# Performance work log

Hardware: AMD Instinct MI355X
Metric: run time of the kernel (lower is better)

Reference implementation:

```python
import jax, jax.numpy as jnp
import numpy as np

V, D, C, H = 32, 128, 2048, 8
B, M = 8, 2048
HD = D // H


def rms_norm(x, scale):
    # Whole-tensor (per-batch) RMS over dims (1,2), as in the source (quirky but faithful).
    Bx, Mx, Dx = x.shape
    fr = jnp.sqrt(jnp.sum(x * x, axis=(1, 2))) * (Mx * Dx) ** -0.5  # (B,)
    raw = x / fr[:, None, None]
    return scale[:Mx, :][None, :, :] * raw


def rope_tables(Mx):
    i = jnp.arange(D // 2, dtype=jnp.float32)
    # NOTE: faithful to source: exponent uses (i-1), not i.
    base = jnp.power(10000.0, -2.0 * (i - 1.0) / D)  # (D/2,)
    pos = jnp.arange(Mx, dtype=jnp.float32)
    ang = pos[:, None] * base[None, :]  # (M, D/2)
    return jnp.cos(ang), jnp.sin(ang)


def apply_rope(t, cos, sin):
    # Equivalent to bmm with the block-diagonal 2x2 rotation matrices:
    # out[2i]   =  t[2i]*cos + t[2i+1]*sin
    # out[2i+1] = -t[2i]*sin + t[2i+1]*cos
    te, to = t[..., 0::2], t[..., 1::2]
    oe = te * cos + to * sin
    oo = -te * sin + to * cos
    return jnp.stack([oe, oo], axis=-1).reshape(t.shape)


def mha(q, k, v, in_w, in_b, out_w, out_b):
    Bx, Mx, _ = q.shape
    qp = q @ in_w[:D].T + in_b[:D]
    kp = k @ in_w[D:2 * D].T + in_b[D:2 * D]
    vp = v @ in_w[2 * D:].T + in_b[2 * D:]
    qh = qp.reshape(Bx, Mx, H, HD).transpose(0, 2, 1, 3)
    kh = kp.reshape(Bx, Mx, H, HD).transpose(0, 2, 1, 3)
    vh = vp.reshape(Bx, Mx, H, HD).transpose(0, 2, 1, 3)
    scores = jnp.einsum('bhqd,bhkd->bhqk', qh, kh) / jnp.sqrt(jnp.float32(HD))
    causal = jnp.tril(jnp.ones((Mx, Mx), dtype=bool))
    scores = jnp.where(causal[None, None], scores, -jnp.inf)
    probs = jax.nn.softmax(scores, axis=-1)  # dropout=0.1 in train mode; eval here
    o = jnp.einsum('bhqk,bhkd->bhqd', probs, vh)
    o = o.transpose(0, 2, 1, 3).reshape(Bx, Mx, D)
    return o @ out_w.T + out_b


def setup_inputs():
    key = jax.random.key(0)
    ks = jax.random.split(key, 12)
    s = 0.02
    return {
        'idx': jax.random.randint(ks[0], (B, M), 0, V),
        'targets': jax.random.randint(ks[1], (B, M), 0, V),
        'emb': jax.random.normal(ks[2], (V, D), jnp.float32) * s,
        'rms_scale': jnp.ones((C, D), jnp.float32),
        'Wq': jax.random.normal(ks[3], (D, D), jnp.float32) * s,
        'Wk': jax.random.normal(ks[4], (D, D), jnp.float32) * s,
        'Wv': jax.random.normal(ks[5], (D, D), jnp.float32) * s,
        'in_proj_w': jax.random.normal(ks[6], (3 * D, D), jnp.float32) * s,
        'in_proj_b': jnp.zeros((3 * D,), jnp.float32),
        'out_proj_w': jax.random.normal(ks[7], (D, D), jnp.float32) * s,
        'out_proj_b': jnp.zeros((D,), jnp.float32),
        'lin_w': jax.random.normal(ks[8], (D, D), jnp.float32) * s,
        'lin_b': jnp.zeros((D,), jnp.float32),
        'out_w': jax.random.normal(ks[9], (V, D), jnp.float32) * s,
        'out_b': jnp.zeros((V,), jnp.float32),
    }


def reference(idx, targets, emb, rms_scale, Wq, Wk, Wv, in_proj_w, in_proj_b,
              out_proj_w, out_proj_b, lin_w, lin_b, out_w, out_b):
    x = emb[idx]                                  # (B, M, D)
    x = rms_norm(x, rms_scale)
    Q = x @ Wq.T
    K = x @ Wk.T
    Vv = x @ Wv.T
    cos, sin = rope_tables(x.shape[1])
    q_out = apply_rope(Q, cos, sin)
    k_out = apply_rope(K, cos, sin)
    v_out = apply_rope(Vv, cos, sin)              # source rotates V too (faithful)
    x = x + mha(q_out, k_out, v_out, in_proj_w, in_proj_b, out_proj_w, out_proj_b)
    x = rms_norm(x, rms_scale)
    x = x + jax.nn.relu(x @ lin_w.T + lin_b)
    logits = x @ out_w.T + out_b                  # (B, M, V)
    logp = jax.nn.log_softmax(logits, axis=-1)
    nll = -jnp.take_along_axis(logp, targets[..., None], axis=-1)[..., 0]
    loss = jnp.mean(nll)
    return logits, loss
```

## Files before the change

kernel.cpp:

```cpp
#include <hip/hip_runtime.h>
#include <hip/hip_bf16.h>
#include <math.h>

#define Vv   32
#define Dd   128
#define Hh   8
#define Bb   8
#define Mm   2048
#define BM   (Bb*Mm)
#define NEL  (BM*Dd)
#define XNS  140
#define QKS  396

typedef _Float16 half4_t __attribute__((ext_vector_type(4)));
typedef _Float16 half8_t __attribute__((ext_vector_type(8)));
typedef __fp16   fp16x2  __attribute__((ext_vector_type(2)));
typedef float    float4_t __attribute__((ext_vector_type(4)));
#define MFMA16 __builtin_amdgcn_mfma_f32_16x16x16f16

#if __has_builtin(__builtin_amdgcn_exp2f)
__device__ __forceinline__ float fexp2(float x) { return __builtin_amdgcn_exp2f(x); }
#else
__device__ __forceinline__ float fexp2(float x) { return __expf(x * 0.6931471805599453f); }
#endif

__global__ __launch_bounds__(256) void prep_kernel(const float* __restrict__ Wq,
                                                   const float* __restrict__ Wk,
                                                   const float* __restrict__ Wv,
                                                   const float* __restrict__ in_w,
                                                   const float* __restrict__ out_pw,
                                                   const float* __restrict__ lin_w,
                                                   const float* __restrict__ out_w,
                                                   _Float16* __restrict__ Wh,
                                                   float* __restrict__ cosT,
                                                   float* __restrict__ sinT) {
    int gid = blockIdx.x * 256 + threadIdx.x;
    if (gid < 135168) {
        const float* src;
        int i;
        if (gid < 131072) {
            int seg = gid >> 14; i = gid & 16383;
            src = seg == 0 ? Wq : seg == 1 ? Wk : seg == 2 ? Wv :
                  seg < 6 ? in_w + (size_t)(seg - 3) * 16384 :
                  seg == 6 ? out_pw : lin_w;
        } else { src = out_w; i = gid - 131072; }
        int tile = i >> 8, within = i & 255;
        int nt = tile >> 3, kk = tile & 7;
        int r = within >> 4, cc = within & 15;
        Wh[gid] = (_Float16)src[(nt * 16 + r) * 128 + kk * 16 + cc];
    } else {
        int rid = gid - 135168;
        int i = rid & 63, m = rid >> 6;
        float ex = -2.0f * ((float)i - 1.0f) / 128.0f;
        float basef = expf(ex * 9.210340371976184f);
        float ang = (float)m * basef;
        cosT[rid] = cosf(ang);
        sinT[rid] = sinf(ang);
    }
}

__global__ __launch_bounds__(256) void gather_sumsq_kernel(const int* __restrict__ idx,
                                                           const float* __restrict__ emb,
                                                           _Float16* __restrict__ Xh,
                                                           float* __restrict__ partials) {
    int gid = blockIdx.x * 256 + threadIdx.x;
    int token = gid >> 5, t4 = gid & 31;
    float4 x = *(const float4*)(emb + (size_t)idx[token] * 128 + t4 * 4);
    half4_t o;
    o[0] = (_Float16)x.x; o[1] = (_Float16)x.y; o[2] = (_Float16)x.z; o[3] = (_Float16)x.w;
    *(half4_t*)(Xh + (size_t)gid * 4) = o;
    float v = x.x * x.x + x.y * x.y + x.z * x.z + x.w * x.w;
    #pragma unroll
    for (int off = 32; off; off >>= 1) v += __shfl_xor(v, off);
    __shared__ float wsum[4];
    int lane = threadIdx.x & 63, wave = threadIdx.x >> 6;
    if (lane == 0) wsum[wave] = v;
    __syncthreads();
    if (threadIdx.x == 0) partials[blockIdx.x] = wsum[0] + wsum[1] + wsum[2] + wsum[3];
}

__global__ __launch_bounds__(256) void normscale_f_kernel(const float* __restrict__ X,
                                                          const float* __restrict__ scale,
                                                          const float* __restrict__ part2,
                                                          _Float16* __restrict__ outh) {
    int gid = blockIdx.x * 256 + threadIdx.x;
    int b = gid >> 16;
    float pv = part2[b * 64 + (threadIdx.x & 63)];
    #pragma unroll
    for (int off = 32; off; off >>= 1) pv += __shfl_xor(pv, off);
    float iv = 512.0f / sqrtf(pv);
    const float* sp = scale + (size_t)((gid >> 5) & 2047) * 128 + (gid & 31) * 4;
    float4 s4 = *(const float4*)sp;
    float4 x = *(const float4*)(X + (size_t)gid * 4);
    half4_t o;
    o[0] = (_Float16)(x.x * iv * s4.x);
    o[1] = (_Float16)(x.y * iv * s4.y);
    o[2] = (_Float16)(x.z * iv * s4.z);
    o[3] = (_Float16)(x.w * iv * s4.w);
    *(half4_t*)(outh + (size_t)gid * 4) = o;
}

__global__ __launch_bounds__(256) void gemm_qkvproj_kernel(const _Float16* __restrict__ xh,
                                                           const float* __restrict__ scale,
                                                           const float* __restrict__ part1,
                                                           const _Float16* __restrict__ Whqkv,
                                                           const _Float16* __restrict__ Whin,
                                                           const float* __restrict__ in_b,
                                                           const float* __restrict__ cosT,
                                                           const float* __restrict__ sinT,
                                                           _Float16* __restrict__ xnh,
                                                           _Float16* __restrict__ Qp,
                                                           _Float16* __restrict__ Kp,
                                                           _Float16* __restrict__ Vp) {
    __shared__ _Float16 xn[32 * XNS];
    __shared__ _Float16 qkv[32 * QKS];
    __shared__ float wsum0[4];
    int tid = threadIdx.x;
    int row0 = blockIdx.x * 32;
    {
        float v = part1[(row0 >> 11) * 256 + tid];
        #pragma unroll
        for (int off = 32; off; off >>= 1) v += __shfl_xor(v, off);
        if ((tid & 63) == 0) wsum0[tid >> 6] = v;
    }
    __syncthreads();
    float iv = 512.0f / sqrtf(wsum0[0] + wsum0[1] + wsum0[2] + wsum0[3]);
    {
        #pragma unroll
        for (int it = 0; it < 2; it++) {
            int idx = tid + it * 256;
            int rw = idx >> 4, c8 = (idx & 15) * 8;
            int m = (row0 + rw) & (Mm - 1);
            half8_t x8 = *(const half8_t*)(xh + (size_t)(row0 + rw) * 128 + c8);
            const float* sp = scale + (size_t)m * 128 + c8;
            float4 s0 = *(const float4*)sp;
            float4 s1 = *(const float4*)(sp + 4);
            half8_t o8;
            o8[0] = (_Float16)((float)x8[0] * iv * s0.x);
            o8[1] = (_Float16)((float)x8[1] * iv * s0.y);
            o8[2] = (_Float16)((float)x8[2] * iv * s0.z);
            o8[3] = (_Float16)((float)x8[3] * iv * s0.w);
            o8[4] = (_Float16)((float)x8[4] * iv * s1.x);
            o8[5] = (_Float16)((float)x8[5] * iv * s1.y);
            o8[6] = (_Float16)((float)x8[6] * iv * s1.z);
            o8[7] = (_Float16)((float)x8[7] * iv * s1.w);
            *(half8_t*)(xn + rw * XNS + c8) = o8;
            *(half8_t*)(xnh + (size_t)(row0 + rw) * 128 + c8) = o8;
        }
    }
    __syncthreads();
    int wave = tid >> 6, lane = tid & 63;
    int r = lane & 15, c = lane >> 4;
    int lofs = r * 16 + 4 * c;
    int nb = wave * 96;
    int nb16 = wave * 6;
    {
        half4_t af[2][8];
        #pragma unroll
        for (int rt = 0; rt < 2; rt++)
            #pragma unroll
            for (int kk = 0; kk < 8; kk++)
                af[rt][kk] = *(const half4_t*)(xn + (rt * 16 + r) * XNS + kk * 16 + 4 * c);
        float4_t acc[2][6];
        #pragma unroll
        for (int rt = 0; rt < 2; rt++)
            #pragma unroll
            for (int t = 0; t < 6; t++) acc[rt][t] = (float4_t){0.f, 0.f, 0.f, 0.f};
        #pragma unroll
        for (int kk = 0; kk < 8; kk++) {
            half4_t wf[6];
            #pragma unroll
            for (int t = 0; t < 6; t++)
                wf[t] = *(const half4_t*)(Whqkv + ((nb16 + t) * 8 + kk) * 256 + lofs);
            #pragma unroll
            for (int t = 0; t < 6; t++) {
                acc[0][t] = MFMA16(af[0][kk], wf[t], acc[0][t], 0, 0, 0);
                acc[1][t] = MFMA16(af[1][kk], wf[t], acc[1][t], 0, 0, 0);
            }
        }
        #pragma unroll
        for (int rt = 0; rt < 2; rt++) {
            #pragma unroll
            for (int t = 0; t < 6; t++) {
                int n = nb + t * 16 + r;
                int ci = (n & 127) >> 1;
                #pragma unroll
                for (int reg = 0; reg < 4; reg++) {
                    int m2 = (row0 + rt * 16 + 4 * c + reg) & (Mm - 1);
                    float v = acc[rt][t][reg];
                    float vp = __shfl_xor(v, 1);
                    float cs = cosT[m2 * 64 + ci], sn = sinT[m2 * 64 + ci];
                    v = (n & 1) ? (-vp * sn + v * cs) : (v * cs + vp * sn);
                    qkv[(rt * 16 + 4 * c + reg) * QKS + n] = (_Float16)v;
                }
            }
        }
    }
    __syncthreads();
    {
        int seg_lo = nb >> 7;
        int seg_hi = (nb + 80) >> 7;
        half4_t aql[2][8], aqh[2][8];
        #pragma unroll
        for (int rt = 0; rt < 2; rt++)
            #pragma unroll
            for (int kk = 0; kk < 8; kk++) {
                aql[rt][kk] = *(const half4_t*)(qkv + (rt * 16 + r) * QKS + seg_lo * 128 + kk * 16 + 4 * c);
                aqh[rt][kk] = *(const half4_t*)(qkv + (rt * 16 + r) * QKS + seg_hi * 128 + kk * 16 + 4 * c);
            }
        float4_t acc[2][6];
        #pragma unroll
        for (int rt = 0; rt < 2; rt++)
            #pragma unroll
            for (int t = 0; t < 6; t++) acc[rt][t] = (float4_t){0.f, 0.f, 0.f, 0.f};
        #pragma unroll
        for (int kk = 0; kk < 8; kk++) {
            half4_t wf[6];
            #pragma unroll
            for (int t = 0; t < 6; t++) {
                int colg = nb + t * 16;
                int seg = colg >> 7;
                int ntl = (colg & 127) >> 4;
                wf[t] = *(const half4_t*)(Whin + ((seg * 8 + ntl) * 8 + kk) * 256 + lofs);
            }
            #pragma unroll
            for (int t = 0; t < 6; t++) {
                int seg = (nb + t * 16) >> 7;
                acc[0][t] = MFMA16(seg == seg_lo ? aql[0][kk] : aqh[0][kk], wf[t], acc[0][t], 0, 0, 0);
                acc[1][t] = MFMA16(seg == seg_lo ? aql[1][kk] : aqh[1][kk], wf[t], acc[1][t], 0, 0, 0);
            }
        }
        int bb = row0 >> 11;
        #pragma unroll
        for (int rt = 0; rt < 2; rt++) {
            int t16 = ((row0 + rt * 16) & 2047) >> 4;
            #pragma unroll
            for (int t = 0; t < 6; t++) {
                int colg = nb + t * 16;
                int seg = colg >> 7;
                int h = (colg & 127) >> 4;
                size_t tb = ((size_t)(bb * 8 + h) * 128 + t16) * 256;
                float bv = in_b[colg + r];
                _Float16* dst = seg == 0 ? Qp : seg == 1 ? Kp : Vp;
                #pragma unroll
                for (int reg = 0; reg < 4; reg++) {
                    float v = acc[rt][t][reg] + bv;
                    int key = 4 * c + reg;
                    if (seg < 2) dst[tb + key * 16 + r] = (_Float16)v;
                    else         dst[tb + r * 16 + key] = (_Float16)v;
                }
            }
        }
    }
}

__global__ __launch_bounds__(256) void gemm_ep1_kernel(const _Float16* __restrict__ Oh,
                                                       const _Float16* __restrict__ W6,
                                                       const float* __restrict__ bias,
                                                       const _Float16* __restrict__ xnh,
                                                       float* __restrict__ xres,
                                                       float* __restrict__ partials) {
    __shared__ _Float16 At[32 * XNS];
    int tid = threadIdx.x;
    int row0 = blockIdx.x * 32;
    #pragma unroll
    for (int it = 0; it < 2; it++) {
        int idx = tid + it * 256;
        int rw = idx >> 4, c8 = (idx & 15) * 8;
        *(half8_t*)(At + rw * XNS + c8) = *(const half8_t*)(Oh + (size_t)(row0 + rw) * 128 + c8);
    }
    __syncthreads();
    int wave = tid >> 6, lane = tid & 63;
    int r = lane & 15, c = lane >> 4;
    int lofs = r * 16 + 4 * c;
    int n0 = wave * 32;
    half4_t af[2][8];
    #pragma unroll
    for (int rt = 0; rt < 2; rt++)
        #pragma unroll
        for (int kk = 0; kk < 8; kk++)
            af[rt][kk] = *(const half4_t*)(At + (rt * 16 + r) * XNS + kk * 16 + 4 * c);
    float4_t acc[2][2];
    #pragma unroll
    for (int rt = 0; rt < 2; rt++) {
        acc[rt][0] = (float4_t){0.f, 0.f, 0.f, 0.f};
        acc[rt][1] = (float4_t){0.f, 0.f, 0.f, 0.f};
    }
    #pragma unroll
    for (int kk = 0; kk < 8; kk++) {
        half4_t wf[2];
        wf[0] = *(const half4_t*)(W6 + ((wave * 2 + 0) * 8 + kk) * 256 + lofs);
        wf[1] = *(const half4_t*)(W6 + ((wave * 2 + 1) * 8 + kk) * 256 + lofs);
        #pragma unroll
        for (int t = 0; t < 2; t++) {
            acc[0][t] = MFMA16(af[0][kk], wf[t], acc[0][t], 0, 0, 0);
            acc[1][t] = MFMA16(af[1][kk], wf[t], acc[1][t], 0, 0, 0);
        }
    }
    float lssq = 0.f;
    #pragma unroll
    for (int rt = 0; rt < 2; rt++) {
        #pragma unroll
        for (int t = 0; t < 2; t++) {
            int n = n0 + t * 16 + r;
            float bv = bias[n];
            #pragma unroll
            for (int reg = 0; reg < 4; reg++) {
                int row = row0 + rt * 16 + 4 * c + reg;
                float v = acc[rt][t][reg] + bv + (float)xnh[(size_t)row * 128 + n];
                lssq += v * v;
                xres[(size_t)row * 128 + n] = v;
            }
        }
    }
    #pragma unroll
    for (int off = 32; off; off >>= 1) lssq += __shfl_xor(lssq, off);
    __shared__ float wsum[4];
    if (lane == 0) wsum[wave] = lssq;
    __syncthreads();
    if (tid == 0) partials[blockIdx.x] = wsum[0] + wsum[1] + wsum[2] + wsum[3];
}

__global__ __launch_bounds__(256) void gemm_ep2_kernel(const _Float16* __restrict__ Ah,
                                                       const _Float16* __restrict__ W7,
                                                       const float* __restrict__ bias,
                                                       const float* __restrict__ xres,
                                                       _Float16* __restrict__ ffoh) {
    __shared__ _Float16 At[32 * XNS];
    int tid = threadIdx.x;
    int row0 = blockIdx.x * 32;
    #pragma unroll
    for (int it = 0; it < 2; it++) {
        int idx = tid + it * 256;
        int rw = idx >> 4, c8 = (idx & 15) * 8;
        *(half8_t*)(At + rw * XNS + c8) = *(const half8_t*)(Ah + (size_t)(row0 + rw) * 128 + c8);
    }
    __syncthreads();
    int wave = tid >> 6, lane = tid & 63;
    int r = lane & 15, c = lane >> 4;
    int lofs = r * 16 + 4 * c;
    int n0 = wave * 32;
    half4_t af[2][8];
    #pragma unroll
    for (int rt = 0; rt < 2; rt++)
        #pragma unroll
        for (int kk = 0; kk < 8; kk++)
            af[rt][kk] = *(const half4_t*)(At + (rt * 16 + r) * XNS + kk * 16 + 4 * c);
    float4_t acc[2][2];
    #pragma unroll
    for (int rt = 0; rt < 2; rt++) {
        acc[rt][0] = (float4_t){0.f, 0.f, 0.f, 0.f};
        acc[rt][1] = (float4_t){0.f, 0.f, 0.f, 0.f};
    }
    #pragma unroll
    for (int kk = 0; kk < 8; kk++) {
        half4_t wf[2];
        wf[0] = *(const half4_t*)(W7 + ((wave * 2 + 0) * 8 + kk) * 256 + lofs);
        wf[1] = *(const half4_t*)(W7 + ((wave * 2 + 1) * 8 + kk) * 256 + lofs);
        #pragma unroll
        for (int t = 0; t < 2; t++) {
            acc[0][t] = MFMA16(af[0][kk], wf[t], acc[0][t], 0, 0, 0);
            acc[1][t] = MFMA16(af[1][kk], wf[t], acc[1][t], 0, 0, 0);
        }
    }
    #pragma unroll
    for (int rt = 0; rt < 2; rt++) {
        #pragma unroll
        for (int t = 0; t < 2; t++) {
            int n = n0 + t * 16 + r;
            float bv = bias[n];
            #pragma unroll
            for (int reg = 0; reg < 4; reg++) {
                int row = row0 + rt * 16 + 4 * c + reg;
                float v = fmaxf(acc[rt][t][reg] + bv, 0.f) + xres[(size_t)row * 128 + n];
                ffoh[(size_t)row * 128 + n] = (_Float16)v;
            }
        }
    }
}

__device__ __forceinline__ half4_t attn_exps(float4_t st, float& ls) {
    float p0 = fexp2(st[0]), p1 = fexp2(st[1]);
    float p2 = fexp2(st[2]), p3 = fexp2(st[3]);
    ls += (p0 + p1) + (p2 + p3);
    fp16x2 lo = __builtin_amdgcn_cvt_pkrtz(p0, p1);
    fp16x2 hi = __builtin_amdgcn_cvt_pkrtz(p2, p3);
    half4_t pf;
    pf[0] = (_Float16)lo[0]; pf[1] = (_Float16)lo[1];
    pf[2] = (_Float16)hi[0]; pf[3] = (_Float16)hi[1];
    return pf;
}
__device__ __forceinline__ half4_t attn_exps_masked(float4_t st, float& ls, int r, int c) {
    float p0 = (4 * c + 0 <= r) ? fexp2(st[0]) : 0.f;
    float p1 = (4 * c + 1 <= r) ? fexp2(st[1]) : 0.f;
    float p2 = (4 * c + 2 <= r) ? fexp2(st[2]) : 0.f;
    float p3 = (4 * c + 3 <= r) ? fexp2(st[3]) : 0.f;
    ls += (p0 + p1) + (p2 + p3);
    fp16x2 lo = __builtin_amdgcn_cvt_pkrtz(p0, p1);
    fp16x2 hi = __builtin_amdgcn_cvt_pkrtz(p2, p3);
    half4_t pf;
    pf[0] = (_Float16)lo[0]; pf[1] = (_Float16)lo[1];
    pf[2] = (_Float16)hi[0]; pf[3] = (_Float16)hi[1];
    return pf;
}

__global__ __launch_bounds__(256) void attn_kernel(const _Float16* __restrict__ Qp,
                                                   const _Float16* __restrict__ Kp,
                                                   const _Float16* __restrict__ Vp,
                                                   _Float16* __restrict__ Oh) {
    __shared__ float mrg[2][10][64];
    int wave = threadIdx.x >> 6, lane = threadIdx.x & 63;
    int pair = blockIdx.x * 2 + (wave >> 1);
    int split = wave & 1;
    int qa = pair & 63, bh = pair >> 6, qb = 127 - qa;
    int r = lane & 15, c = lane >> 4;
    int lofs = r * 16 + 4 * c;
    const _Float16* Kb = Kp + (size_t)bh * 32768 + lofs;
    const _Float16* Vb = Vp + (size_t)bh * 32768 + lofs;
    const _Float16* Qb = Qp + (size_t)bh * 32768 + lofs;
    half4_t qfa = *(const half4_t*)(Qb + qa * 256);
    half4_t qfb = *(const half4_t*)(Qb + qb * 256);
    const _Float16 qscale = (_Float16)0.36067376f;
    qfa *= qscale;
    qfb *= qscale;
    float4_t zero = {0.f, 0.f, 0.f, 0.f};
    float4_t oa = zero, ob = zero;
    float lsa = 0.f, lsb = 0.f;

    for (int kt = split; kt < qa; kt += 2) {
        half4_t k0 = *(const half4_t*)(Kb + (size_t)kt * 256);
        half4_t v0 = *(const half4_t*)(Vb + (size_t)kt * 256);
        float4_t sa = MFMA16(k0, qfa, zero, 0, 0, 0);
        float4_t sb = MFMA16(k0, qfb, zero, 0, 0, 0);
        half4_t pa = attn_exps(sa, lsa);
        half4_t pb = attn_exps(sb, lsb);
        oa = MFMA16(pa, v0, oa, 0, 0, 0);
        ob = MFMA16(pb, v0, ob, 0, 0, 0);
    }
    if ((qa & 1) == split) {
        half4_t k0 = *(const half4_t*)(Kb + (size_t)qa * 256);
        half4_t v0 = *(const half4_t*)(Vb + (size_t)qa * 256);
        float4_t sa = MFMA16(k0, qfa, zero, 0, 0, 0);
        float4_t sb = MFMA16(k0, qfb, zero, 0, 0, 0);
        half4_t pa = attn_exps_masked(sa, lsa, r, c);
        half4_t pb = attn_exps(sb, lsb);
        oa = MFMA16(pa, v0, oa, 0, 0, 0);
        ob = MFMA16(pb, v0, ob, 0, 0, 0);
    }
    {
        int s = qa + 1;
        if ((s & 1) != split) s++;
        for (int kt = s; kt < qb; kt += 2) {
            half4_t k0 = *(const half4_t*)(Kb + (size_t)kt * 256);
            half4_t v0 = *(const half4_t*)(Vb + (size_t)kt * 256);
            float4_t sb = MFMA16(k0, qfb, zero, 0, 0, 0);
            half4_t pb = attn_exps(sb, lsb);
            ob = MFMA16(pb, v0, ob, 0, 0, 0);
        }
    }
    if ((qb & 1) == split) {
        half4_t k0 = *(const half4_t*)(Kb + (size_t)qb * 256);
        half4_t v0 = *(const half4_t*)(Vb + (size_t)qb * 256);
        float4_t sb = MFMA16(k0, qfb, zero, 0, 0, 0);
        half4_t pb = attn_exps_masked(sb, lsb, r, c);
        ob = MFMA16(pb, v0, ob, 0, 0, 0);
    }
    int pib = wave >> 1;
    if (split == 1) {
        #pragma unroll
        for (int i = 0; i < 4; i++) {
            mrg[pib][i][lane] = oa[i];
            mrg[pib][4 + i][lane] = ob[i];
        }
        mrg[pib][8][lane] = lsa;
        mrg[pib][9][lane] = lsb;
    }
    __syncthreads();
    if (split == 0) {
        #pragma unroll
        for (int i = 0; i < 4; i++) {
            oa[i] += mrg[pib][i][lane];
            ob[i] += mrg[pib][4 + i][lane];
        }
        lsa += mrg[pib][8][lane];
        lsb += mrg[pib][9][lane];
        lsa += __shfl_xor(lsa, 16); lsa += __shfl_xor(lsa, 32);
        lsb += __shfl_xor(lsb, 16); lsb += __shfl_xor(lsb, 32);
        int b = bh >> 3, h = bh & 7;
        #pragma unroll
        for (int reg = 0; reg < 4; reg++) {
            float la = __shfl(lsa, 4 * c + reg);
            float lb = __shfl(lsb, 4 * c + reg);
            Oh[(size_t)(b * Mm + qa * 16 + 4 * c + reg) * 128 + h * 16 + r] = (_Float16)(oa[reg] / la);
            Oh[(size_t)(b * Mm + qb * 16 + 4 * c + reg) * 128 + h * 16 + r] = (_Float16)(ob[reg] / lb);
        }
    }
}

__global__ __launch_bounds__(256) void logits_loss_kernel(const _Float16* __restrict__ Xh,
                                                          const _Float16* __restrict__ Wo16,
                                                          const float* __restrict__ bo,
                                                          const int* __restrict__ targets,
                                                          float* __restrict__ logits,
                                                          float* __restrict__ nllBuf) {
    __shared__ _Float16 At[64 * XNS];
    int tid = threadIdx.x;
    int rowb = blockIdx.x * 64;
    #pragma unroll
    for (int it = 0; it < 4; it++) {
        int idx = tid + it * 256;
        int rw = idx >> 4, c8 = (idx & 15) * 8;
        *(half8_t*)(At + rw * XNS + c8) = *(const half8_t*)(Xh + (size_t)(rowb + rw) * 128 + c8);
    }
    __syncthreads();
    int wave = tid >> 6, lane = tid & 63;
    int r = lane & 15, c = lane >> 4;
    int lofs = r * 16 + 4 * c;
    int row0 = rowb + wave * 16;
    half4_t af[8];
    #pragma unroll
    for (int kk = 0; kk < 8; kk++)
        af[kk] = *(const half4_t*)(At + (wave * 16 + r) * XNS + kk * 16 + 4 * c);
    float4_t acc[2];
    acc[0] = (float4_t){0.f, 0.f, 0.f, 0.f};
    acc[1] = (float4_t){0.f, 0.f, 0.f, 0.f};
    #pragma unroll
    for (int kk = 0; kk < 8; kk++) {
        #pragma unroll
        for (int t = 0; t < 2; t++) {
            half4_t wf = *(const half4_t*)(Wo16 + (t * 8 + kk) * 256 + lofs);
            acc[t] = MFMA16(af[kk], wf, acc[t], 0, 0, 0);
        }
    }
    float b0 = bo[r], b1 = bo[r + 16];
    #pragma unroll
    for (int reg = 0; reg < 4; reg++) {
        int row = row0 + 4 * c + reg;
        float l0 = acc[0][reg] + b0;
        float l1 = acc[1][reg] + b1;
        logits[(size_t)row * 32 + r] = l0;
        logits[(size_t)row * 32 + 16 + r] = l1;
        float mx = fmaxf(l0, l1);
        #pragma unroll
        for (int off = 8; off; off >>= 1) mx = fmaxf(mx, __shfl_xor(mx, off));
        float se = __expf(l0 - mx) + __expf(l1 - mx);
        #pragma unroll
        for (int off = 8; off; off >>= 1) se += __shfl_xor(se, off);
        int tgt = targets[row];
        float sel = (tgt & 16) ? l1 : l0;
        float tval = __shfl(sel, (lane & 48) | (tgt & 15));
        if (r == 0) nllBuf[row] = logf(se) + mx - tval;
    }
}

__global__ __launch_bounds__(256) void loss_reduce_kernel(const float* __restrict__ nllBuf,
                                                          float* __restrict__ out) {
    int t = threadIdx.x;
    double s = 0.0;
    #pragma unroll
    for (int i = 0; i < 64; i++) s += (double)nllBuf[t * 64 + i];
    __shared__ double sh[256];
    sh[t] = s;
    __syncthreads();
    for (int off = 128; off; off >>= 1) {
        if (t < off) sh[t] += sh[t + off];
        __syncthreads();
    }
    if (t == 0) out[0] = (float)(sh[0] * (1.0 / (double)BM));
}

extern "C" void kernel_launch(void* const* d_in, const int* in_sizes, int n_in,
                              void* d_out, int out_size, void* d_ws, size_t ws_size,
                              hipStream_t stream) {
    const int*   idx       = (const int*)d_in[0];
    const int*   targets   = (const int*)d_in[1];
    const float* emb       = (const float*)d_in[2];
    const float* rms_scale = (const float*)d_in[3];
    const float* Wq        = (const float*)d_in[4];
    const float* Wk        = (const float*)d_in[5];
    const float* Wv        = (const float*)d_in[6];
    const float* in_w      = (const float*)d_in[7];
    const float* in_b      = (const float*)d_in[8];
    const float* out_pw    = (const float*)d_in[9];
    const float* out_pb    = (const float*)d_in[10];
    const float* lin_w     = (const float*)d_in[11];
    const float* lin_b     = (const float*)d_in[12];
    const float* out_w     = (const float*)d_in[13];
    const float* out_b     = (const float*)d_in[14];
    float* out = (float*)d_out;

    char* base = (char*)d_ws;
    const size_t MB = 1024 * 1024;
    _Float16* xh16  = (_Float16*)base;
    _Float16* xnh   = (_Float16*)(base + 4 * MB);
    _Float16* Oh    = (_Float16*)(base + 8 * MB);
    _Float16* x2nh  = (_Float16*)(base + 12 * MB);
    _Float16* ffoh  = (_Float16*)(base + 16 * MB);
    _Float16* Qp    = (_Float16*)(base + 20 * MB);
    _Float16* Kp    = (_Float16*)(base + 24 * MB);
    _Float16* Vp    = (_Float16*)(base + 28 * MB);
    float*    xres  = (float*)(base + 32 * MB);
    float*    cosT  = (float*)(base + 40 * MB);
    float*    sinT  = cosT + Mm * 64;
    float*    part1 = sinT + Mm * 64;
    float*    part2 = part1 + 2048;
    _Float16* Wh    = (_Float16*)(part2 + 512);
    float*    nllBuf = (float*)(Wh + 135168);

    prep_kernel<<<1040, 256, 0, stream>>>(Wq, Wk, Wv, in_w, out_pw, lin_w, out_w, Wh, cosT, sinT);
    gather_sumsq_kernel<<<NEL / 1024, 256, 0, stream>>>(idx, emb, xh16, part1);

    gemm_qkvproj_kernel<<<BM / 32, 256, 0, stream>>>(xh16, rms_scale, part1,
                                                     Wh, Wh + 3 * 16384, in_b,
                                                     cosT, sinT, xnh, Qp, Kp, Vp);

    attn_kernel<<<4096 / 2, 256, 0, stream>>>(Qp, Kp, Vp, Oh);

    gemm_ep1_kernel<<<BM / 32, 256, 0, stream>>>(Oh, Wh + 6 * 16384, out_pb, xnh, xres, part2);
    normscale_f_kernel<<<NEL / 1024, 256, 0, stream>>>(xres, rms_scale, part2, x2nh);
    gemm_ep2_kernel<<<BM / 32, 256, 0, stream>>>(x2nh, Wh + 7 * 16384, lin_b, xres, ffoh);

    logits_loss_kernel<<<BM / 64, 256, 0, stream>>>(ffoh, Wh + 131072, out_b, targets, out, nllBuf);
    loss_reduce_kernel<<<1, 256, 0, stream>>>(nllBuf, out + (size_t)BM * Vv);
}
```

Measured before the change: 169.0 us.

## Fuse prep with embedding gather and fold second RMS norm into FFN GEMM

Combines the weight-conversion/rope-table kernel and the embedding gather/sum-of-squares kernel into a single launch by dispatching on block index. Removes the standalone normalize-and-scale kernel by having the FFN GEMM read the fp32 residual directly, compute the per-batch inverse RMS and apply the scale while staging A into shared memory. This saves two kernel launches and a write/read of an intermediate fp16 activation buffer, at the cost of the GEMM reading fp32 data and scale rows instead of fp16.

```diff
diff --git a/kernel.cpp b/kernel.cpp
--- a/kernel.cpp
+++ b/kernel.cpp
@@ -24,80 +24,61 @@
 __device__ __forceinline__ float fexp2(float x) { return __expf(x * 0.6931471805599453f); }
 #endif
 
-__global__ __launch_bounds__(256) void prep_kernel(const float* __restrict__ Wq,
-                                                   const float* __restrict__ Wk,
-                                                   const float* __restrict__ Wv,
-                                                   const float* __restrict__ in_w,
-                                                   const float* __restrict__ out_pw,
-                                                   const float* __restrict__ lin_w,
-                                                   const float* __restrict__ out_w,
-                                                   _Float16* __restrict__ Wh,
-                                                   float* __restrict__ cosT,
-                                                   float* __restrict__ sinT) {
-    int gid = blockIdx.x * 256 + threadIdx.x;
-    if (gid < 135168) {
-        const float* src;
-        int i;
-        if (gid < 131072) {
-            int seg = gid >> 14; i = gid & 16383;
-            src = seg == 0 ? Wq : seg == 1 ? Wk : seg == 2 ? Wv :
-                  seg < 6 ? in_w + (size_t)(seg - 3) * 16384 :
-                  seg == 6 ? out_pw : lin_w;
-        } else { src = out_w; i = gid - 131072; }
-        int tile = i >> 8, within = i & 255;
-        int nt = tile >> 3, kk = tile & 7;
-        int r = within >> 4, cc = within & 15;
-        Wh[gid] = (_Float16)src[(nt * 16 + r) * 128 + kk * 16 + cc];
+__global__ __launch_bounds__(256) void front_kernel(const float* __restrict__ Wq,
+                                                    const float* __restrict__ Wk,
+                                                    const float* __restrict__ Wv,
+                                                    const float* __restrict__ in_w,
+                                                    const float* __restrict__ out_pw,
+                                                    const float* __restrict__ lin_w,
+                                                    const float* __restrict__ out_w,
+                                                    _Float16* __restrict__ Wh,
+                                                    float* __restrict__ cosT,
+                                                    float* __restrict__ sinT,
+                                                    const int* __restrict__ idx,
+                                                    const float* __restrict__ emb,
+                                                    _Float16* __restrict__ Xh,
+                                                    float* __restrict__ partials) {
+    __shared__ float wsum[4];
+    if (blockIdx.x < 1040) {
+        int gid = blockIdx.x * 256 + threadIdx.x;
+        if (gid < 135168) {
+            const float* src;
+            int i;
+            if (gid < 131072) {
+                int seg = gid >> 14; i = gid & 16383;
+                src = seg == 0 ? Wq : seg == 1 ? Wk : seg == 2 ? Wv :
+                      seg < 6 ? in_w + (size_t)(seg - 3) * 16384 :
+                      seg == 6 ? out_pw : lin_w;
+            } else { src = out_w; i = gid - 131072; }
+            int tile = i >> 8, within = i & 255;
+            int nt = tile >> 3, kk = tile & 7;
+            int r = within >> 4, cc = within & 15;
+            Wh[gid] = (_Float16)src[(nt * 16 + r) * 128 + kk * 16 + cc];
+        } else {
+            int rid = gid - 135168;
+            int i = rid & 63, m = rid >> 6;
+            float ex = -2.0f * ((float)i - 1.0f) / 128.0f;
+            float basef = expf(ex * 9.210340371976184f);
+            float ang = (float)m * basef;
+            cosT[rid] = cosf(ang);
+            sinT[rid] = sinf(ang);
+        }
     } else {
-        int rid = gid - 135168;
-        int i = rid & 63, m = rid >> 6;
-        float ex = -2.0f * ((float)i - 1.0f) / 128.0f;
-        float basef = expf(ex * 9.210340371976184f);
-        float ang = (float)m * basef;
-        cosT[rid] = cosf(ang);
-        sinT[rid] = sinf(ang);
-    }
-}
-
-__global__ __launch_bounds__(256) void gather_sumsq_kernel(const int* __restrict__ idx,
-                                                           const float* __restrict__ emb,
-                                                           _Float16* __restrict__ Xh,
-                                                           float* __restrict__ partials) {
-    int gid = blockIdx.x * 256 + threadIdx.x;
-    int token = gid >> 5, t4 = gid & 31;
-    float4 x = *(const float4*)(emb + (size_t)idx[token] * 128 + t4 * 4);
-    half4_t o;
-    o[0] = (_Float16)x.x; o[1] = (_Float16)x.y; o[2] = (_Float16)x.z; o[3] = (_Float16)x.w;
-    *(half4_t*)(Xh + (size_t)gid * 4) = o;
-    float v = x.x * x.x + x.y * x.y + x.z * x.z + x.w * x.w;
-    #pragma unroll
-    for (int off = 32; off; off >>= 1) v += __shfl_xor(v, off);
-    __shared__ float wsum[4];
-    int lane = threadIdx.x & 63, wave = threadIdx.x >> 6;
-    if (lane == 0) wsum[wave] = v;
-    __syncthreads();
-    if (threadIdx.x == 0) partials[blockIdx.x] = wsum[0] + wsum[1] + wsum[2] + wsum[3];
-}
-
-__global__ __launch_bounds__(256) void normscale_f_kernel(const float* __restrict__ X,
-                                                          const float* __restrict__ scale,
-                                                          const float* __restrict__ part2,
-                                                          _Float16* __restrict__ outh) {
-    int gid = blockIdx.x * 256 + threadIdx.x;
-    int b = gid >> 16;
-    float pv = part2[b * 64 + (threadIdx.x & 63)];
-    #pragma unroll
-    for (int off = 32; off; off >>= 1) pv += __shfl_xor(pv, off);
-    float iv = 512.0f / sqrtf(pv);
-    const float* sp = scale + (size_t)((gid >> 5) & 2047) * 128 + (gid & 31) * 4;
-    float4 s4 = *(const float4*)sp;
-    float4 x = *(const float4*)(X + (size_t)gid * 4);
-    half4_t o;
-    o[0] = (_Float16)(x.x * iv * s4.x);
-    o[1] = (_Float16)(x.y * iv * s4.y);
-    o[2] = (_Float16)(x.z * iv * s4.z);
-    o[3] = (_Float16)(x.w * iv * s4.w);
-    *(half4_t*)(outh + (size_t)gid * 4) = o;
+        int blk = blockIdx.x - 1040;
+        int gid = blk * 256 + threadIdx.x;
+        int token = gid >> 5, t4 = gid & 31;
+        float4 x = *(const float4*)(emb + (size_t)idx[token] * 128 + t4 * 4);
+        half4_t o;
+        o[0] = (_Float16)x.x; o[1] = (_Float16)x.y; o[2] = (_Float16)x.z; o[3] = (_Float16)x.w;
+        *(half4_t*)(Xh + (size_t)gid * 4) = o;
+        float v = x.x * x.x + x.y * x.y + x.z * x.z + x.w * x.w;
+        #pragma unroll
+        for (int off = 32; off; off >>= 1) v += __shfl_xor(v, off);
+        int lane = threadIdx.x & 63, wave = threadIdx.x >> 6;
+        if (lane == 0) wsum[wave] = v;
+        __syncthreads();
+        if (threadIdx.x == 0) partials[blk] = wsum[0] + wsum[1] + wsum[2] + wsum[3];
+    }
 }
 
 __global__ __launch_bounds__(256) void gemm_qkvproj_kernel(const _Float16* __restrict__ xh,
@@ -321,19 +302,40 @@
     if (tid == 0) partials[blockIdx.x] = wsum[0] + wsum[1] + wsum[2] + wsum[3];
 }
 
-__global__ __launch_bounds__(256) void gemm_ep2_kernel(const _Float16* __restrict__ Ah,
+__global__ __launch_bounds__(256) void gemm_ep2_kernel(const float* __restrict__ xres,
+                                                       const float* __restrict__ scale,
+                                                       const float* __restrict__ part2,
                                                        const _Float16* __restrict__ W7,
                                                        const float* __restrict__ bias,
-                                                       const float* __restrict__ xres,
                                                        _Float16* __restrict__ ffoh) {
     __shared__ _Float16 At[32 * XNS];
     int tid = threadIdx.x;
     int row0 = blockIdx.x * 32;
+    float pv = part2[(row0 >> 11) * 64 + (tid & 63)];
+    #pragma unroll
+    for (int off = 32; off; off >>= 1) pv += __shfl_xor(pv, off);
+    float iv = 512.0f / sqrtf(pv);
     #pragma unroll
     for (int it = 0; it < 2; it++) {
         int idx = tid + it * 256;
         int rw = idx >> 4, c8 = (idx & 15) * 8;
-        *(half8_t*)(At + rw * XNS + c8) = *(const half8_t*)(Ah + (size_t)(row0 + rw) * 128 + c8);
+        int m = (row0 + rw) & (Mm - 1);
+        const float* xp = xres + (size_t)(row0 + rw) * 128 + c8;
+        float4 x0 = *(const float4*)xp;
+        float4 x1 = *(const float4*)(xp + 4);
+        const float* sp = scale + (size_t)m * 128 + c8;
+        float4 s0 = *(const float4*)sp;
+        float4 s1 = *(const float4*)(sp + 4);
+        half8_t o8;
+        o8[0] = (_Float16)(x0.x * iv * s0.x);
+        o8[1] = (_Float16)(x0.y * iv * s0.y);
+        o8[2] = (_Float16)(x0.z * iv * s0.z);
+        o8[3] = (_Float16)(x0.w * iv * s0.w);
+        o8[4] = (_Float16)(x1.x * iv * s1.x);
+        o8[5] = (_Float16)(x1.y * iv * s1.y);
+        o8[6] = (_Float16)(x1.z * iv * s1.z);
+        o8[7] = (_Float16)(x1.w * iv * s1.w);
+        *(half8_t*)(At + rw * XNS + c8) = o8;
     }
     __syncthreads();
     int wave = tid >> 6, lane = tid & 63;
@@ -594,7 +596,6 @@
     _Float16* xh16  = (_Float16*)base;
     _Float16* xnh   = (_Float16*)(base + 4 * MB);
     _Float16* Oh    = (_Float16*)(base + 8 * MB);
-    _Float16* x2nh  = (_Float16*)(base + 12 * MB);
     _Float16* ffoh  = (_Float16*)(base + 16 * MB);
     _Float16* Qp    = (_Float16*)(base + 20 * MB);
     _Float16* Kp    = (_Float16*)(base + 24 * MB);
@@ -607,8 +608,8 @@
     _Float16* Wh    = (_Float16*)(part2 + 512);
     float*    nllBuf = (float*)(Wh + 135168);
 
-    prep_kernel<<<1040, 256, 0, stream>>>(Wq, Wk, Wv, in_w, out_pw, lin_w, out_w, Wh, cosT, sinT);
-    gather_sumsq_kernel<<<NEL / 1024, 256, 0, stream>>>(idx, emb, xh16, part1);
+    front_kernel<<<1040 + 2048, 256, 0, stream>>>(Wq, Wk, Wv, in_w, out_pw, lin_w, out_w,
+                                                  Wh, cosT, sinT, idx, emb, xh16, part1);
 
     gemm_qkvproj_kernel<<<BM / 32, 256, 0, stream>>>(xh16, rms_scale, part1,
                                                      Wh, Wh + 3 * 16384, in_b,
@@ -617,8 +618,7 @@
     attn_kernel<<<4096 / 2, 256, 0, stream>>>(Qp, Kp, Vp, Oh);
 
     gemm_ep1_kernel<<<BM / 32, 256, 0, stream>>>(Oh, Wh + 6 * 16384, out_pb, xnh, xres, part2);
-    normscale_f_kernel<<<NEL / 1024, 256, 0, stream>>>(xres, rms_scale, part2, x2nh);
-    gemm_ep2_kernel<<<BM / 32, 256, 0, stream>>>(x2nh, Wh + 7 * 16384, lin_b, xres, ffoh);
+    gemm_ep2_kernel<<<BM / 32, 256, 0, stream>>>(xres, rms_scale, part2, Wh + 7 * 16384, lin_b, ffoh);
 
     logits_loss_kernel<<<BM / 64, 256, 0, stream>>>(ffoh, Wh + 131072, out_b, targets, out, nllBuf);
     loss_reduce_kernel<<<1, 256, 0, stream>>>(nllBuf, out + (size_t)BM * Vv);
```

After: 167.0 us. About the same (-1.2%).
